# Performance work log

Hardware: AMD Instinct MI355X
Metric: run time of the kernel (lower is better)

Reference implementation:

```python
import jax, jax.numpy as jnp
import numpy as np
import math

N = 8192
D = 512

def setup_inputs() -> dict:
    key = jax.random.key(0)
    k1, k2, k3, k4, k5 = jax.random.split(key, 5)
    x = jax.random.normal(k1, (N, D), dtype=jnp.float32)
    mask = jax.random.randint(k2, (N, N), 0, 2) == 1
    s = 1.0 / math.sqrt(D)
    Wq = jax.random.normal(k3, (D, D), dtype=jnp.float32) * s
    Wk = jax.random.normal(k4, (D, D), dtype=jnp.float32) * s
    Wv = jax.random.normal(k5, (D, D), dtype=jnp.float32) * s
    return {"x": x, "mask": mask, "Wq": Wq, "Wk": Wk, "Wv": Wv}

def reference(x, mask, Wq, Wk, Wv):
    d_model = x.shape[-1]
    # torch nn.Linear: y = x @ W^T
    Q = x @ Wq.T
    K = x @ Wk.T
    V = x @ Wv.T
    scores = (Q @ K.T) / jnp.sqrt(jnp.asarray(d_model, x.dtype))  # [N, N]
    scores = jnp.where(mask, jnp.asarray(-1e9, x.dtype), scores)
    # manual stable softmax, matching the original op sequence
    scores = jnp.exp(scores - jnp.max(scores, axis=1, keepdims=True))
    attn = scores / jnp.sum(scores, axis=-1, keepdims=True)
    cntx = attn @ V
    return (cntx, attn)
```

## Files before the change

kernel.cpp:

```cpp
#include <hip/hip_runtime.h>

#define NTOK 8192
#define DMODEL 512
#define NWORDS 128
#define ESTRIDE (2 * NTOK)

typedef _Float16 f16;
typedef _Float16 f16x4 __attribute__((ext_vector_type(4)));
typedef _Float16 f16x8 __attribute__((ext_vector_type(8)));
typedef float f32x4 __attribute__((ext_vector_type(4)));
typedef unsigned long long u64;

__device__ __forceinline__ void async_ld16(const void* g, void* l) {
  __builtin_amdgcn_global_load_lds((const __attribute__((address_space(1))) void*)g,
                                   (__attribute__((address_space(3))) void*)l, 16, 0, 0);
}

__global__ void pack_f16(const float* __restrict__ s, f16* __restrict__ d, int n) {
  int i = (blockIdx.x * 256 + threadIdx.x) * 4;
  if (i >= n) return;
  float4 v = *(const float4*)(s + i);
  f16x4 h; h.x = (f16)v.x; h.y = (f16)v.y; h.z = (f16)v.z; h.w = (f16)v.w;
  *(f16x4*)(d + i) = h;
}

__global__ __launch_bounds__(256) void pack_mask(const int* __restrict__ mask,
                                                 u64* __restrict__ bits) {
  int wave = (blockIdx.x * 256 + threadIdx.x) >> 6;
  int lane = threadIdx.x & 63;
  size_t W0 = (size_t)wave * 8;
#pragma unroll
  for (int i = 0; i < 8; ++i) {
    int m = mask[(W0 + i) * 64 + lane];
    u64 b = __ballot(m != 0);
    if (lane == 0) bits[W0 + i] = b;
  }
}

__global__ __launch_bounds__(256) void transpose_f16(const f16* __restrict__ src,
                                                     f16* __restrict__ dst) {
  __shared__ f16 T[64][72];
  int t = threadIdx.x;
  int tok0 = blockIdx.x * 64, d0 = blockIdx.y * 64;
#pragma unroll
  for (int i = 0; i < 2; ++i) {
    int row = (t >> 3) + i * 32;
    int col = (t & 7) * 8;
    f16x8 v = *(const f16x8*)(src + (size_t)(tok0 + row) * DMODEL + d0 + col);
    *(f16x8*)(&T[row][col]) = v;
  }
  __syncthreads();
#pragma unroll
  for (int i = 0; i < 2; ++i) {
    int od = (t >> 3) + i * 32;
    int ot = (t & 7) * 8;
    f16x8 v;
#pragma unroll
    for (int j = 0; j < 8; ++j) v[j] = T[ot + j][od];
    *(f16x8*)(dst + (size_t)(d0 + od) * NTOK + tok0 + ot) = v;
  }
}

__device__ __forceinline__ void stage128x64(const f16* G, int r0, int k0, int rs,
                                            f16* lds, int t) {
  int wv = t >> 6;
  int sw = (((t & 7) ^ ((t >> 3) & 7)) * 8);
  const f16* g = G + (size_t)(r0 + (t >> 3)) * rs + k0 + sw;
#pragma unroll
  for (int i = 0; i < 4; ++i)
    async_ld16(g + (size_t)i * 32 * rs, (char*)lds + i * 4096 + wv * 1024);
}

template <int RS>
__device__ __forceinline__ void gemm128(const f16* A, const f16* B, int m0, int n0,
                                        f16* As, f16* Bs, int t, f32x4 (&acc)[4][4]) {
  int lane = t & 63, wv = t >> 6, quad = lane >> 4, l15 = lane & 15;
  int m_off = (wv & 1) * 64, n_off = (wv >> 1) * 64;
  for (int kt = 0; kt < RS; kt += 64) {
    __syncthreads();
    stage128x64(A, m0, kt, RS, As, t);
    stage128x64(B, n0, kt, RS, Bs, t);
    __syncthreads();
#pragma unroll
    for (int ks = 0; ks < 2; ++ks) {
      int sl = (((ks << 2) | quad) ^ (l15 & 7)) * 8;
      f16x8 af[4], bf[4];
#pragma unroll
      for (int mt = 0; mt < 4; ++mt)
        af[mt] = *(const f16x8*)(As + (m_off + mt * 16 + l15) * 64 + sl);
#pragma unroll
      for (int nt = 0; nt < 4; ++nt)
        bf[nt] = *(const f16x8*)(Bs + (n_off + nt * 16 + l15) * 64 + sl);
#pragma unroll
      for (int mt = 0; mt < 4; ++mt)
#pragma unroll
        for (int nt = 0; nt < 4; ++nt)
          acc[mt][nt] = __builtin_amdgcn_mfma_f32_16x16x32_f16(af[mt], bf[nt], acc[mt][nt], 0, 0, 0);
    }
  }
}

__global__ __launch_bounds__(256) void qkv_gemm(const f16* __restrict__ X,
                                                const f16* __restrict__ Wall,
                                                f16* __restrict__ Out) {
  __shared__ f16 As[128 * 64];
  __shared__ f16 Bs[128 * 64];
  int t = threadIdx.x;
  int z = blockIdx.z;
  const f16* B = Wall + (size_t)z * DMODEL * DMODEL;
  f16* C = Out + (size_t)z * NTOK * DMODEL;
  int m0 = blockIdx.y * 128, n0 = blockIdx.x * 128;
  int lane = t & 63, wv = t >> 6, quad = lane >> 4, l15 = lane & 15;
  int m_off = (wv & 1) * 64, n_off = (wv >> 1) * 64;
  f32x4 acc[4][4] = {};
  gemm128<DMODEL>(X, B, m0, n0, As, Bs, t, acc);
#pragma unroll
  for (int mt = 0; mt < 4; ++mt)
#pragma unroll
    for (int nt = 0; nt < 4; ++nt)
#pragma unroll
      for (int r = 0; r < 4; ++r) {
        int row = m0 + m_off + mt * 16 + quad * 4 + r;
        int col = n0 + n_off + nt * 16 + l15;
        C[(size_t)row * DMODEL + col] = (f16)acc[mt][nt][r];
      }
}

__global__ __launch_bounds__(256) void scores2(const f16* __restrict__ Q,
                                               const f16* __restrict__ Kh,
                                               const u64* __restrict__ bits,
                                               f16* __restrict__ Eh,
                                               float* __restrict__ rowsum) {
  __shared__ f16 SM[128 * 128];
  f16* As = SM;
  f16* Bs = SM + 128 * 64;
  int t = threadIdx.x;
  int m0 = blockIdx.y * 128, n0 = blockIdx.x * 128;
  int lane = t & 63, wv = t >> 6, quad = lane >> 4, l15 = lane & 15;
  int m_off = (wv & 1) * 64, n_off = (wv >> 1) * 64;
  f32x4 acc[4][4] = {};
  gemm128<DMODEL>(Q, Kh, m0, n0, As, Bs, t, acc);
  const float scale = 0.044194173824159216f;
  __syncthreads();
#pragma unroll
  for (int mt = 0; mt < 4; ++mt)
#pragma unroll
    for (int r = 0; r < 4; ++r) {
      int lrow = m_off + mt * 16 + quad * 4 + r;
      int row = m0 + lrow;
      u64 w = bits[(size_t)row * NWORDS + ((n0 + n_off) >> 6)];
      float rs = 0.f;
#pragma unroll
      for (int nt = 0; nt < 4; ++nt) {
        float s = acc[mt][nt][r] * scale;
        float e = ((w >> (nt * 16 + l15)) & 1) ? 0.f : __expf(s);
        rs += e;
        int col = n_off + nt * 16 + l15;
        int phys = (((col >> 3) ^ (lrow & 15)) << 3) | (col & 7);
        SM[lrow * 128 + phys] = (f16)e;
      }
      rs += __shfl_xor(rs, 1);
      rs += __shfl_xor(rs, 2);
      rs += __shfl_xor(rs, 4);
      rs += __shfl_xor(rs, 8);
      if (l15 == 0) atomicAdd(&rowsum[row], rs);
    }
  __syncthreads();
#pragma unroll
  for (int p = 0; p < 8; ++p) {
    int lrow = p * 16 + (t >> 4);
    int cb = t & 15;
    f16x8 v = *(const f16x8*)(SM + lrow * 128 + ((cb ^ (lrow & 15)) << 3));
    *(f16x8*)(Eh + (size_t)(m0 + lrow) * ESTRIDE + n0 + cb * 8) = v;
  }
}

__global__ __launch_bounds__(512, 2) void pv_kernel(const f16* __restrict__ Eh,
                                                    const float* __restrict__ rowsum,
                                                    const f16* __restrict__ Vt,
                                                    float* __restrict__ cntx) {
  __shared__ f16 Es[128 * 64];
  __shared__ f16 Vs[512 * 64];
  int t = threadIdx.x;
  int r0 = blockIdx.x * 128;
  int k0 = blockIdx.y * 2048;
  int lane = t & 63, wv = t >> 6, quad = lane >> 4, l15 = lane & 15;
  int m_off = (wv & 1) * 64, n_off = (wv >> 1) * 128;
  int sw = (((t & 7) ^ ((t >> 3) & 7)) * 8);
  f32x4 acc[4][8] = {};
  for (int kt = k0; kt < k0 + 2048; kt += 64) {
    __syncthreads();
#pragma unroll
    for (int i = 0; i < 2; ++i)
      async_ld16(Eh + (size_t)(r0 + i * 64 + (t >> 3)) * ESTRIDE + kt + sw,
                 (char*)Es + i * 8192 + wv * 1024);
#pragma unroll
    for (int i = 0; i < 8; ++i)
      async_ld16(Vt + (size_t)(i * 64 + (t >> 3)) * NTOK + kt + sw,
                 (char*)Vs + i * 8192 + wv * 1024);
    __syncthreads();
#pragma unroll
    for (int ks = 0; ks < 2; ++ks) {
      int sl = (((ks << 2) | quad) ^ (l15 & 7)) * 8;
      f16x8 af[4], bf[8];
#pragma unroll
      for (int mt = 0; mt < 4; ++mt)
        af[mt] = *(const f16x8*)(Es + (m_off + mt * 16 + l15) * 64 + sl);
#pragma unroll
      for (int nt = 0; nt < 8; ++nt)
        bf[nt] = *(const f16x8*)(Vs + (n_off + nt * 16 + l15) * 64 + sl);
#pragma unroll
      for (int mt = 0; mt < 4; ++mt)
#pragma unroll
        for (int nt = 0; nt < 8; ++nt)
          acc[mt][nt] = __builtin_amdgcn_mfma_f32_16x16x32_f16(af[mt], bf[nt], acc[mt][nt], 0, 0, 0);
    }
  }
#pragma unroll
  for (int mt = 0; mt < 4; ++mt)
#pragma unroll
    for (int r = 0; r < 4; ++r) {
      int row = r0 + m_off + mt * 16 + quad * 4 + r;
      float ri = 1.0f / rowsum[row];
#pragma unroll
      for (int nt = 0; nt < 8; ++nt) {
        int col = n_off + nt * 16 + l15;
        atomicAdd(&cntx[(size_t)row * DMODEL + col], acc[mt][nt][r] * ri);
      }
    }
}

__global__ __launch_bounds__(256) void expand_attn(float* __restrict__ attn,
                                                   const float* __restrict__ rowsum) {
  __shared__ f16 B[4][8192];
  int t = threadIdx.x;
  int wv = t >> 6, lane = t & 63;
  int row = blockIdx.x * 4 + wv;
  const f16* src = (const f16*)(attn + (size_t)row * NTOK);
#pragma unroll
  for (int i = 0; i < 16; ++i)
    async_ld16(src + i * 512 + lane * 8, (char*)&B[wv][0] + i * 1024);
  __syncthreads();
  float ri = 1.0f / rowsum[row];
  float* dst = attn + (size_t)row * NTOK;
#pragma unroll
  for (int c = 0; c < NTOK; c += 512) {
    f16x8 v = *(const f16x8*)(&B[wv][c + lane * 8]);
    float4 lo, hi;
    lo.x = (float)v[0] * ri; lo.y = (float)v[1] * ri;
    lo.z = (float)v[2] * ri; lo.w = (float)v[3] * ri;
    hi.x = (float)v[4] * ri; hi.y = (float)v[5] * ri;
    hi.z = (float)v[6] * ri; hi.w = (float)v[7] * ri;
    *(float4*)(dst + c + lane * 8) = lo;
    *(float4*)(dst + c + lane * 8 + 4) = hi;
  }
}

extern "C" void kernel_launch(void* const* d_in, const int* in_sizes, int n_in,
                              void* d_out, int out_size, void* d_ws, size_t ws_size,
                              hipStream_t stream) {
  const float* x  = (const float*)d_in[0];
  const int* mask = (const int*)d_in[1];
  const float* Wq = (const float*)d_in[2];
  const float* Wk = (const float*)d_in[3];
  const float* Wv = (const float*)d_in[4];
  float* cntx = (float*)d_out;
  float* attn = (float*)d_out + (size_t)NTOK * DMODEL;

  f16* xh = (f16*)d_ws;
  f16* Wh = xh + (size_t)NTOK * DMODEL;
  f16* QKV = Wh + (size_t)3 * DMODEL * DMODEL;
  f16* Qh = QKV;
  f16* Kh = QKV + (size_t)NTOK * DMODEL;
  f16* Vh = QKV + (size_t)2 * NTOK * DMODEL;
  f16* Vt = QKV + (size_t)3 * NTOK * DMODEL;
  float* rowsum = (float*)(Vt + (size_t)NTOK * DMODEL);

  u64* bits = (u64*)cntx;
  f16* Eh = (f16*)attn;

  hipMemsetAsync(rowsum, 0, NTOK * sizeof(float), stream);

  pack_f16<<<dim3(NTOK * DMODEL / 1024), 256, 0, stream>>>(x, xh, NTOK * DMODEL);
  pack_f16<<<dim3(DMODEL * DMODEL / 1024), 256, 0, stream>>>(Wq, Wh, DMODEL * DMODEL);
  pack_f16<<<dim3(DMODEL * DMODEL / 1024), 256, 0, stream>>>(Wk, Wh + DMODEL * DMODEL, DMODEL * DMODEL);
  pack_f16<<<dim3(DMODEL * DMODEL / 1024), 256, 0, stream>>>(Wv, Wh + 2 * DMODEL * DMODEL, DMODEL * DMODEL);
  pack_mask<<<dim3(NTOK * NWORDS / 8 / 4), 256, 0, stream>>>(mask, bits);

  qkv_gemm<<<dim3(DMODEL / 128, NTOK / 128, 3), 256, 0, stream>>>(xh, Wh, QKV);
  transpose_f16<<<dim3(NTOK / 64, DMODEL / 64), 256, 0, stream>>>(Vh, Vt);
  scores2<<<dim3(NTOK / 128, NTOK / 128), 256, 0, stream>>>(Qh, Kh, bits, Eh, rowsum);

  hipMemsetAsync(cntx, 0, (size_t)NTOK * DMODEL * sizeof(float), stream);
  pv_kernel<<<dim3(NTOK / 128, 4), 512, 0, stream>>>(Eh, rowsum, Vt, cntx);
  expand_attn<<<dim3(NTOK / 4), 256, 0, stream>>>(attn, rowsum);
}
```

Baseline: 852.2 us.

## Double-buffer GEMM and PV staging, swizzle block order, stream attn expansion

The shared GEMM helper and the PV kernel now use double-buffered LDS stages. The next K tile is fetched asynchronously while the current one feeds the MFMAs, which removes one barrier per iteration and hides global-load latency. The PV K-step drops to 32 to fit two buffers. The scores and PV kernels remap block indices into grouped orders to improve L2 reuse of shared rows and columns. The mask, E and attn streams use nontemporal loads and stores, and expand_attn keeps each row in registers instead of LDS. These changes raise LDS footprint, and the in-place register expansion relies on every load finishing before the overlapping stores.

```diff
diff --git a/kernel.cpp b/kernel.cpp
--- a/kernel.cpp
+++ b/kernel.cpp
@@ -31,7 +31,7 @@
   size_t W0 = (size_t)wave * 8;
 #pragma unroll
   for (int i = 0; i < 8; ++i) {
-    int m = mask[(W0 + i) * 64 + lane];
+    int m = __builtin_nontemporal_load(mask + (W0 + i) * 64 + lane);
     u64 b = __ballot(m != 0);
     if (lane == 0) bits[W0 + i] = b;
   }
@@ -74,37 +74,44 @@
 template <int RS>
 __device__ __forceinline__ void gemm128(const f16* A, const f16* B, int m0, int n0,
                                         f16* As, f16* Bs, int t, f32x4 (&acc)[4][4]) {
-  int lane = t & 63, wv = t >> 6, quad = lane >> 4, l15 = lane & 15;
+  int lane = t & 63, quad = lane >> 4, l15 = lane & 15, wv = t >> 6;
   int m_off = (wv & 1) * 64, n_off = (wv >> 1) * 64;
+  stage128x64(A, m0, 0, RS, As, t);
+  stage128x64(B, n0, 0, RS, Bs, t);
+  __syncthreads();
   for (int kt = 0; kt < RS; kt += 64) {
-    __syncthreads();
-    stage128x64(A, m0, kt, RS, As, t);
-    stage128x64(B, n0, kt, RS, Bs, t);
-    __syncthreads();
+    int cur = (kt >> 6) & 1;
+    if (kt + 64 < RS) {
+      stage128x64(A, m0, kt + 64, RS, As + (cur ^ 1) * 8192, t);
+      stage128x64(B, n0, kt + 64, RS, Bs + (cur ^ 1) * 8192, t);
+    }
+    const f16* Ac = As + cur * 8192;
+    const f16* Bc = Bs + cur * 8192;
 #pragma unroll
     for (int ks = 0; ks < 2; ++ks) {
       int sl = (((ks << 2) | quad) ^ (l15 & 7)) * 8;
       f16x8 af[4], bf[4];
 #pragma unroll
       for (int mt = 0; mt < 4; ++mt)
-        af[mt] = *(const f16x8*)(As + (m_off + mt * 16 + l15) * 64 + sl);
+        af[mt] = *(const f16x8*)(Ac + (m_off + mt * 16 + l15) * 64 + sl);
 #pragma unroll
       for (int nt = 0; nt < 4; ++nt)
-        bf[nt] = *(const f16x8*)(Bs + (n_off + nt * 16 + l15) * 64 + sl);
+        bf[nt] = *(const f16x8*)(Bc + (n_off + nt * 16 + l15) * 64 + sl);
 #pragma unroll
       for (int mt = 0; mt < 4; ++mt)
 #pragma unroll
         for (int nt = 0; nt < 4; ++nt)
           acc[mt][nt] = __builtin_amdgcn_mfma_f32_16x16x32_f16(af[mt], bf[nt], acc[mt][nt], 0, 0, 0);
     }
+    __syncthreads();
   }
 }
 
 __global__ __launch_bounds__(256) void qkv_gemm(const f16* __restrict__ X,
                                                 const f16* __restrict__ Wall,
                                                 f16* __restrict__ Out) {
-  __shared__ f16 As[128 * 64];
-  __shared__ f16 Bs[128 * 64];
+  __shared__ f16 As[2 * 128 * 64];
+  __shared__ f16 Bs[2 * 128 * 64];
   int t = threadIdx.x;
   int z = blockIdx.z;
   const f16* B = Wall + (size_t)z * DMODEL * DMODEL;
@@ -131,17 +138,19 @@
                                                const u64* __restrict__ bits,
                                                f16* __restrict__ Eh,
                                                float* __restrict__ rowsum) {
-  __shared__ f16 SM[128 * 128];
+  __shared__ f16 SM[2 * 128 * 128];
   f16* As = SM;
-  f16* Bs = SM + 128 * 64;
-  int t = threadIdx.x;
-  int m0 = blockIdx.y * 128, n0 = blockIdx.x * 128;
+  f16* Bs = SM + 16384;
+  int t = threadIdx.x;
+  int orig = blockIdx.x + (blockIdx.y << 6);
+  int wg = (orig & 7) * 512 + (orig >> 3);
+  int m0 = (((wg >> 9) * 8 + (wg & 7))) * 128;
+  int n0 = ((wg >> 3) & 63) * 128;
   int lane = t & 63, wv = t >> 6, quad = lane >> 4, l15 = lane & 15;
   int m_off = (wv & 1) * 64, n_off = (wv >> 1) * 64;
   f32x4 acc[4][4] = {};
   gemm128<DMODEL>(Q, Kh, m0, n0, As, Bs, t, acc);
   const float scale = 0.044194173824159216f;
-  __syncthreads();
 #pragma unroll
   for (int mt = 0; mt < 4; ++mt)
 #pragma unroll
@@ -171,50 +180,57 @@
     int lrow = p * 16 + (t >> 4);
     int cb = t & 15;
     f16x8 v = *(const f16x8*)(SM + lrow * 128 + ((cb ^ (lrow & 15)) << 3));
-    *(f16x8*)(Eh + (size_t)(m0 + lrow) * ESTRIDE + n0 + cb * 8) = v;
-  }
+    __builtin_nontemporal_store(v, (f16x8*)(Eh + (size_t)(m0 + lrow) * ESTRIDE + n0 + cb * 8));
+  }
+}
+
+__device__ __forceinline__ void stage_pv(const f16* __restrict__ Eh,
+                                         const f16* __restrict__ Vt, int r0, int kt,
+                                         f16* Es, f16* Vs, int t) {
+  int wv = t >> 6;
+  int srcsw = (((t & 3) ^ ((t >> 2) & 3)) * 8);
+  async_ld16(Eh + (size_t)(r0 + (t >> 2)) * ESTRIDE + kt + srcsw, (char*)Es + wv * 1024);
+#pragma unroll
+  for (int i = 0; i < 4; ++i)
+    async_ld16(Vt + (size_t)(i * 128 + (t >> 2)) * NTOK + kt + srcsw,
+               (char*)Vs + i * 8192 + wv * 1024);
 }
 
 __global__ __launch_bounds__(512, 2) void pv_kernel(const f16* __restrict__ Eh,
                                                     const float* __restrict__ rowsum,
                                                     const f16* __restrict__ Vt,
                                                     float* __restrict__ cntx) {
-  __shared__ f16 Es[128 * 64];
-  __shared__ f16 Vs[512 * 64];
-  int t = threadIdx.x;
-  int r0 = blockIdx.x * 128;
-  int k0 = blockIdx.y * 2048;
+  __shared__ f16 Es[2][128 * 32];
+  __shared__ f16 Vs[2][512 * 32];
+  int t = threadIdx.x;
+  int orig = blockIdx.x + (blockIdx.y << 6);
+  int wg = (orig & 7) * 32 + (orig >> 3);
+  int r0 = (wg & 63) * 128;
+  int k0 = (wg >> 6) * 2048;
   int lane = t & 63, wv = t >> 6, quad = lane >> 4, l15 = lane & 15;
   int m_off = (wv & 1) * 64, n_off = (wv >> 1) * 128;
-  int sw = (((t & 7) ^ ((t >> 3) & 7)) * 8);
+  int sl2 = (quad ^ (l15 & 3)) * 8;
   f32x4 acc[4][8] = {};
-  for (int kt = k0; kt < k0 + 2048; kt += 64) {
+  stage_pv(Eh, Vt, r0, k0, Es[0], Vs[0], t);
+  __syncthreads();
+  for (int i = 0; i < 64; ++i) {
+    int cur = i & 1;
+    if (i < 63) stage_pv(Eh, Vt, r0, k0 + (i + 1) * 32, Es[cur ^ 1], Vs[cur ^ 1], t);
+    const f16* Ec = Es[cur];
+    const f16* Vc = Vs[cur];
+    f16x8 af[4], bf[8];
+#pragma unroll
+    for (int mt = 0; mt < 4; ++mt)
+      af[mt] = *(const f16x8*)(Ec + (m_off + mt * 16 + l15) * 32 + sl2);
+#pragma unroll
+    for (int nt = 0; nt < 8; ++nt)
+      bf[nt] = *(const f16x8*)(Vc + (n_off + nt * 16 + l15) * 32 + sl2);
+#pragma unroll
+    for (int mt = 0; mt < 4; ++mt)
+#pragma unroll
+      for (int nt = 0; nt < 8; ++nt)
+        acc[mt][nt] = __builtin_amdgcn_mfma_f32_16x16x32_f16(af[mt], bf[nt], acc[mt][nt], 0, 0, 0);
     __syncthreads();
-#pragma unroll
-    for (int i = 0; i < 2; ++i)
-      async_ld16(Eh + (size_t)(r0 + i * 64 + (t >> 3)) * ESTRIDE + kt + sw,
-                 (char*)Es + i * 8192 + wv * 1024);
-#pragma unroll
-    for (int i = 0; i < 8; ++i)
-      async_ld16(Vt + (size_t)(i * 64 + (t >> 3)) * NTOK + kt + sw,
-                 (char*)Vs + i * 8192 + wv * 1024);
-    __syncthreads();
-#pragma unroll
-    for (int ks = 0; ks < 2; ++ks) {
-      int sl = (((ks << 2) | quad) ^ (l15 & 7)) * 8;
-      f16x8 af[4], bf[8];
-#pragma unroll
-      for (int mt = 0; mt < 4; ++mt)
-        af[mt] = *(const f16x8*)(Es + (m_off + mt * 16 + l15) * 64 + sl);
-#pragma unroll
-      for (int nt = 0; nt < 8; ++nt)
-        bf[nt] = *(const f16x8*)(Vs + (n_off + nt * 16 + l15) * 64 + sl);
-#pragma unroll
-      for (int mt = 0; mt < 4; ++mt)
-#pragma unroll
-        for (int nt = 0; nt < 8; ++nt)
-          acc[mt][nt] = __builtin_amdgcn_mfma_f32_16x16x32_f16(af[mt], bf[nt], acc[mt][nt], 0, 0, 0);
-    }
   }
 #pragma unroll
   for (int mt = 0; mt < 4; ++mt)
@@ -232,28 +248,31 @@
 
 __global__ __launch_bounds__(256) void expand_attn(float* __restrict__ attn,
                                                    const float* __restrict__ rowsum) {
-  __shared__ f16 B[4][8192];
   int t = threadIdx.x;
   int wv = t >> 6, lane = t & 63;
   int row = blockIdx.x * 4 + wv;
+  float ri = 1.0f / rowsum[row];
   const f16* src = (const f16*)(attn + (size_t)row * NTOK);
-#pragma unroll
-  for (int i = 0; i < 16; ++i)
-    async_ld16(src + i * 512 + lane * 8, (char*)&B[wv][0] + i * 1024);
-  __syncthreads();
-  float ri = 1.0f / rowsum[row];
   float* dst = attn + (size_t)row * NTOK;
-#pragma unroll
-  for (int c = 0; c < NTOK; c += 512) {
-    f16x8 v = *(const f16x8*)(&B[wv][c + lane * 8]);
-    float4 lo, hi;
-    lo.x = (float)v[0] * ri; lo.y = (float)v[1] * ri;
-    lo.z = (float)v[2] * ri; lo.w = (float)v[3] * ri;
-    hi.x = (float)v[4] * ri; hi.y = (float)v[5] * ri;
-    hi.z = (float)v[6] * ri; hi.w = (float)v[7] * ri;
-    *(float4*)(dst + c + lane * 8) = lo;
-    *(float4*)(dst + c + lane * 8 + 4) = hi;
-  }
+  f16x8 v0, v1, v2, v3, v4, v5, v6, v7, v8, v9, va, vb, vc, vd, ve, vf;
+#define LD(i, reg) reg = __builtin_nontemporal_load((const f16x8*)(src + (i) * 512 + lane * 8))
+  LD(0, v0); LD(1, v1); LD(2, v2); LD(3, v3); LD(4, v4); LD(5, v5); LD(6, v6); LD(7, v7);
+  LD(8, v8); LD(9, v9); LD(10, va); LD(11, vb); LD(12, vc); LD(13, vd); LD(14, ve); LD(15, vf);
+#undef LD
+  asm volatile("" ::: "memory");
+#define ST(i, reg)                                                            \
+  {                                                                           \
+    f32x4 lo, hi;                                                             \
+    lo.x = (float)reg[0] * ri; lo.y = (float)reg[1] * ri;                     \
+    lo.z = (float)reg[2] * ri; lo.w = (float)reg[3] * ri;                     \
+    hi.x = (float)reg[4] * ri; hi.y = (float)reg[5] * ri;                     \
+    hi.z = (float)reg[6] * ri; hi.w = (float)reg[7] * ri;                     \
+    __builtin_nontemporal_store(lo, (f32x4*)(dst + (i) * 512 + lane * 8));    \
+    __builtin_nontemporal_store(hi, (f32x4*)(dst + (i) * 512 + lane * 8 + 4)); \
+  }
+  ST(0, v0); ST(1, v1); ST(2, v2); ST(3, v3); ST(4, v4); ST(5, v5); ST(6, v6); ST(7, v7);
+  ST(8, v8); ST(9, v9); ST(10, va); ST(11, vb); ST(12, vc); ST(13, vd); ST(14, ve); ST(15, vf);
+#undef ST
 }
 
 extern "C" void kernel_launch(void* const* d_in, const int* in_sizes, int n_in,
```

Measured after the change: 899.4 us. 1.06x slower.
